# Optimization experiments

Hardware: AMD Instinct MI355X
Metric: run time of the kernel (lower is better)

The kernel has to match this reference:

```python
import jax, jax.numpy as jnp
import numpy as np

B, N, F_ = 4, 2048, 512
H = 8
D = F_ // H


def setup_inputs() -> dict:
    key = jax.random.key(0)
    ks = jax.random.split(key, 9)
    s = 1.0 / np.sqrt(F_)
    return {
        "x": jax.random.normal(ks[0], (B, N, F_), dtype=jnp.float32),
        "Wq": jax.random.normal(ks[1], (F_, F_), dtype=jnp.float32) * s,
        "bq": jax.random.normal(ks[2], (F_,), dtype=jnp.float32) * 0.01,
        "Wk": jax.random.normal(ks[3], (F_, F_), dtype=jnp.float32) * s,
        "bk": jax.random.normal(ks[4], (F_,), dtype=jnp.float32) * 0.01,
        "Wv": jax.random.normal(ks[5], (F_, F_), dtype=jnp.float32) * s,
        "bv": jax.random.normal(ks[6], (F_,), dtype=jnp.float32) * 0.01,
        "Wo": jax.random.normal(ks[7], (F_, F_), dtype=jnp.float32) * s,
        "bo": jax.random.normal(ks[8], (F_,), dtype=jnp.float32) * 0.01,
    }


def reference(x, Wq, bq, Wk, bk, Wv, bv, Wo, bo):
    b, n, f = x.shape
    h, d = H, f // H
    # projections -> [b, h, n, d]
    q = (x @ Wq + bq).reshape(b, n, h, d).transpose(0, 2, 1, 3)
    k = (x @ Wk + bk).reshape(b, n, h, d).transpose(0, 2, 1, 3)
    v = (x @ Wv + bv).reshape(b, n, h, d).transpose(0, 2, 1, 3)
    # NOTE: module scales by sqrt(feats), not sqrt(head_dim)
    sqrt_d = jnp.asarray(f, x.dtype) ** 0.5
    score = jax.nn.softmax(jnp.einsum('bhif,bhjf->bhij', q, k) / sqrt_d, axis=-1)
    attn = jnp.einsum('bhij,bhjf->bihf', score, v).reshape(b, n, f)
    return attn @ Wo + bo
```

## Files before the change

### kernel.cpp

```cpp
#include <hip/hip_runtime.h>


typedef _Float16 f16;
typedef _Float16 f16x2 __attribute__((ext_vector_type(2)));
typedef _Float16 f16x4 __attribute__((ext_vector_type(4)));
typedef _Float16 f16x8 __attribute__((ext_vector_type(8)));
typedef float f32x4 __attribute__((ext_vector_type(4)));

#define MFMA16(a, b, c) __builtin_amdgcn_mfma_f32_16x16x32_f16((a), (b), (c), 0, 0, 0)
#if __has_builtin(__builtin_amdgcn_exp2f)
#define EXP2(x) __builtin_amdgcn_exp2f(x)
#else
#define EXP2(x) exp2f(x)
#endif
#define GLLDS16(gp, lp)                                                    \
  __builtin_amdgcn_global_load_lds(                                        \
      (const __attribute__((address_space(1))) unsigned int*)(gp),         \
      (__attribute__((address_space(3))) unsigned int*)(lp), 16, 0, 0)

#define QSCALE 0.0637587f

__global__ __launch_bounds__(256) void k_cvt_x(const float* __restrict__ x,
                                               f16* __restrict__ xb, int n4) {
  int i = blockIdx.x * 256 + threadIdx.x;
  const int stride = gridDim.x * 256;
  const float4* xp = (const float4*)x;
  f16x4* op = (f16x4*)xb;
  for (; i < n4; i += stride) {
    float4 v = xp[i];
    f16x4 o = {(f16)v.x, (f16)v.y, (f16)v.z, (f16)v.w};
    op[i] = o;
  }
}

__global__ __launch_bounds__(256) void k_cvt_w(const float* __restrict__ Wq,
                                               const float* __restrict__ Wk,
                                               const float* __restrict__ Wv,
                                               const float* __restrict__ Wo,
                                               f16* __restrict__ wt) {
  const int w = blockIdx.y;
  const float* W = (w == 0) ? Wq : (w == 1) ? Wk : (w == 2) ? Wv : Wo;
  const int j0 = (blockIdx.x >> 4) * 32;
  const int k0 = (blockIdx.x & 15) * 32;
  __shared__ float tl[32][33];
  const int tx = threadIdx.x & 31, ty = threadIdx.x >> 5;
#pragma unroll
  for (int i = 0; i < 32; i += 8)
    tl[ty + i][tx] = W[(size_t)(k0 + ty + i) * 512 + j0 + tx];
  __syncthreads();
#pragma unroll
  for (int i = 0; i < 32; i += 8)
    wt[(size_t)w * 262144 + (size_t)(j0 + ty + i) * 512 + (k0 + tx)] =
        (f16)tl[tx][ty + i];
}

__global__ __launch_bounds__(256) void k_gemm(
    const f16* __restrict__ A, const f16* __restrict__ Wb3,
    const float* __restrict__ bias0, const float* __restrict__ bias1,
    const float* __restrict__ bias2, f16* __restrict__ oQ, f16* __restrict__ oK,
    f16* __restrict__ oV, float* __restrict__ oOut, int mode) {
  __shared__ __align__(16) f16 a_lds[128 * 64];
  __shared__ __align__(16) f16 b_lds[128 * 64];
  const int t = threadIdx.x;
  const int lane = t & 63, wid = t >> 6;
  const int l15 = lane & 15, l4 = lane >> 4;
  const int wm = wid >> 1, wn = wid & 1;
  const int m0 = blockIdx.x * 128;
  const int by = blockIdx.y;
  const int wsel = (mode == 0) ? (by >> 2) : 0;
  const int n0l = (mode == 0) ? ((by & 3) * 128) : (by * 128);
  const f16* Wt = Wb3 + (size_t)wsel * 262144;

  const int srow = t >> 3;
  const int sslot = t & 7;
  const int sswz = (sslot ^ (srow & 7)) * 8;

  f32x4 acc[4][4];
  const f32x4 z4 = {0.f, 0.f, 0.f, 0.f};
#pragma unroll
  for (int i = 0; i < 4; i++)
#pragma unroll
    for (int j = 0; j < 4; j++) acc[i][j] = z4;

  for (int k0 = 0; k0 < 512; k0 += 64) {
#pragma unroll
    for (int i = 0; i < 4; i++) {
      const int r = i * 32 + srow;
      *(f16x8*)&a_lds[r * 64 + sslot * 8] =
          *(const f16x8*)&A[(size_t)(m0 + r) * 512 + k0 + sswz];
      *(f16x8*)&b_lds[r * 64 + sslot * 8] =
          *(const f16x8*)&Wt[(size_t)(n0l + r) * 512 + k0 + sswz];
    }
    __syncthreads();
#pragma unroll
    for (int ks = 0; ks < 2; ks++) {
      const int rs = ((ks * 4 + l4) ^ (l15 & 7)) * 8;
      f16x8 af[4], bf[4];
#pragma unroll
      for (int mt = 0; mt < 4; mt++)
        af[mt] = *(const f16x8*)&a_lds[(wm * 64 + mt * 16 + l15) * 64 + rs];
#pragma unroll
      for (int nt = 0; nt < 4; nt++)
        bf[nt] = *(const f16x8*)&b_lds[(wn * 64 + nt * 16 + l15) * 64 + rs];
      __builtin_amdgcn_s_setprio(1);
#pragma unroll
      for (int mt = 0; mt < 4; mt++)
#pragma unroll
        for (int nt = 0; nt < 4; nt++)
          acc[mt][nt] = MFMA16(af[mt], bf[nt], acc[mt][nt]);
      __builtin_amdgcn_s_setprio(0);
    }
    __syncthreads();
  }

  if (mode == 1) {
#pragma unroll
    for (int mt = 0; mt < 4; mt++)
#pragma unroll
      for (int nt = 0; nt < 4; nt++) {
        const int row = m0 + wm * 64 + mt * 16 + l4 * 4;
        const int col = n0l + wn * 64 + nt * 16 + l15;
        const float bv = bias0[col];
#pragma unroll
        for (int r = 0; r < 4; r++)
          oOut[(size_t)(row + r) * 512 + col] = acc[mt][nt][r] + bv;
      }
  } else {
#pragma unroll
    for (int mt = 0; mt < 4; mt++)
#pragma unroll
      for (int nt = 0; nt < 4; nt++) {
        const int colg = by * 128 + wn * 64 + nt * 16 + l15;
        const int w = colg >> 9, jj = colg & 511;
        const int h = jj >> 6, d = jj & 63;
        const float* bp = (w == 0) ? bias0 : (w == 1) ? bias1 : bias2;
        const float bv = bp[jj];
        const float scl = (w == 0) ? QSCALE : 1.0f;
        const int rowg = m0 + wm * 64 + mt * 16 + l4 * 4;
        const int b = rowg >> 11, nn = rowg & 2047;
        if (w == 2) {
          const size_t vb = ((size_t)(b * 8 + h) * 64 + d) * 2048 + nn;
#pragma unroll
          for (int r = 0; r < 4; r++)
            oV[vb + r] = (f16)(acc[mt][nt][r] + bv);
        } else {
          f16* op = (w == 0) ? oQ : oK;
          const size_t base = ((size_t)(b * 8 + h) * 2048 + nn) * 64 + d;
#pragma unroll
          for (int r = 0; r < 4; r++)
            op[base + (size_t)r * 64] = (f16)((acc[mt][nt][r] + bv) * scl);
        }
      }
  }
}

__global__ __launch_bounds__(256, 2) void k_attn(const f16* __restrict__ Q,
                                                 const f16* __restrict__ K,
                                                 const f16* __restrict__ Vt,
                                                 f16* __restrict__ CTX) {
  __shared__ __align__(16) f16 k_lds[2][4096];
  __shared__ __align__(16) f16 v_lds[2][4096];
  const int t = threadIdx.x, wid = t >> 6, lane = t & 63;
  const int l15 = lane & 15, l4 = lane >> 4;
  const int bid = blockIdx.x;
  const int bh = (bid & 7) * 4 + (bid >> 7);
  const int qb = (bid >> 3) & 15;
  const int q0 = qb * 128 + wid * 32;
  const size_t kvb = (size_t)bh * (2048 * 64);

  f16x8 qf[2][2];
#pragma unroll
  for (int g = 0; g < 2; g++)
#pragma unroll
    for (int ks = 0; ks < 2; ks++)
      qf[g][ks] = *(const f16x8*)&Q[kvb + (size_t)(q0 + g * 16 + l15) * 64 +
                                    ks * 32 + l4 * 8];

  f32x4 oa[2][4];
  f32x4 lacc[2];
  const f32x4 z4 = {0.f, 0.f, 0.f, 0.f};
#pragma unroll
  for (int g = 0; g < 2; g++) {
    lacc[g] = z4;
#pragma unroll
    for (int dt = 0; dt < 4; dt++) oa[g][dt] = z4;
  }
  const f16 one = (f16)1.0f;
  const f16x8 ones = {one, one, one, one, one, one, one, one};

  const int krow = wid * 8 + (lane >> 3);
  const int kswz = ((lane & 7) ^ (lane >> 3)) * 8;
  const int kperm = ((krow & 0x0C) << 1) | ((krow & 0x10) >> 2) | (krow & 3);
  const f16* Kg = K + kvb + (size_t)kperm * 64 + kswz;
  const f16* Vg = Vt + kvb + (size_t)krow * 2048 + kswz;

  GLLDS16(Kg, &k_lds[0][wid * 512]);
  GLLDS16(Kg + 2048, &k_lds[0][wid * 512 + 2048]);
  GLLDS16(Vg, &v_lds[0][wid * 512]);
  GLLDS16(Vg + 32 * 2048, &v_lds[0][wid * 512 + 2048]);
  __syncthreads();

  int cur = 0;
  for (int it = 0; it < 32; ++it) {
    if (it < 31) {
      const size_t kb = (size_t)(it + 1) * 4096;
      const size_t vb = (size_t)(it + 1) * 64;
      GLLDS16(Kg + kb, &k_lds[cur ^ 1][wid * 512]);
      GLLDS16(Kg + kb + 2048, &k_lds[cur ^ 1][wid * 512 + 2048]);
      GLLDS16(Vg + vb, &v_lds[cur ^ 1][wid * 512]);
      GLLDS16(Vg + vb + 32 * 2048, &v_lds[cur ^ 1][wid * 512 + 2048]);
    }

    f32x4 st[2][4];
#pragma unroll
    for (int g = 0; g < 2; g++)
#pragma unroll
      for (int w = 0; w < 4; w++) st[g][w] = z4;
    const f16* kl = k_lds[cur];
#pragma unroll
    for (int ks = 0; ks < 2; ks++) {
      const int rs = ((ks * 4 + l4) ^ (l15 & 7)) * 8;
      f16x8 kf[4];
#pragma unroll
      for (int w = 0; w < 4; w++)
        kf[w] = *(const f16x8*)&kl[(w * 16 + l15) * 64 + rs];
      __builtin_amdgcn_s_setprio(1);
#pragma unroll
      for (int w = 0; w < 4; w++) {
        st[0][w] = MFMA16(kf[w], qf[0][ks], st[0][w]);
        st[1][w] = MFMA16(kf[w], qf[1][ks], st[1][w]);
      }
      __builtin_amdgcn_s_setprio(0);
    }

    f16x8 pa[2][2];
#pragma unroll
    for (int g = 0; g < 2; g++)
#pragma unroll
      for (int ks = 0; ks < 2; ks++) {
        f16x2 a0 = __builtin_bit_cast(
            f16x2, __builtin_amdgcn_cvt_pkrtz(EXP2(st[g][2 * ks][0]),
                                              EXP2(st[g][2 * ks][1])));
        f16x2 a1 = __builtin_bit_cast(
            f16x2, __builtin_amdgcn_cvt_pkrtz(EXP2(st[g][2 * ks][2]),
                                              EXP2(st[g][2 * ks][3])));
        f16x2 a2 = __builtin_bit_cast(
            f16x2, __builtin_amdgcn_cvt_pkrtz(EXP2(st[g][2 * ks + 1][0]),
                                              EXP2(st[g][2 * ks + 1][1])));
        f16x2 a3 = __builtin_bit_cast(
            f16x2, __builtin_amdgcn_cvt_pkrtz(EXP2(st[g][2 * ks + 1][2]),
                                              EXP2(st[g][2 * ks + 1][3])));
        f16x8 p;
        p[0] = a0[0]; p[1] = a0[1]; p[2] = a1[0]; p[3] = a1[1];
        p[4] = a2[0]; p[5] = a2[1]; p[6] = a3[0]; p[7] = a3[1];
        pa[g][ks] = p;
      }

    const f16* vl = v_lds[cur];
#pragma unroll
    for (int ks = 0; ks < 2; ks++) {
      __builtin_amdgcn_s_setprio(1);
      lacc[0] = MFMA16(pa[0][ks], ones, lacc[0]);
      lacc[1] = MFMA16(pa[1][ks], ones, lacc[1]);
#pragma unroll
      for (int dt = 0; dt < 4; dt++) {
        const f16x8 vf = *(const f16x8*)&vl[(dt * 16 + l15) * 64 +
                                            ((ks * 4 + l4) ^ (l15 & 7)) * 8];
        oa[0][dt] = MFMA16(pa[0][ks], vf, oa[0][dt]);
        oa[1][dt] = MFMA16(pa[1][ks], vf, oa[1][dt]);
      }
      __builtin_amdgcn_s_setprio(0);
    }
    __syncthreads();
    cur ^= 1;
  }

  const int b = bh >> 3, h = bh & 7;
#pragma unroll
  for (int g = 0; g < 2; g++)
#pragma unroll
    for (int r = 0; r < 4; r++) {
      const float inv = 1.0f / lacc[g][r];
      const int qrow = q0 + g * 16 + l4 * 4 + r;
#pragma unroll
      for (int dt = 0; dt < 4; dt++)
        CTX[(size_t)(b * 2048 + qrow) * 512 + h * 64 + dt * 16 + l15] =
            (f16)(oa[g][dt][r] * inv);
    }
}

extern "C" void kernel_launch(void* const* d_in, const int* in_sizes, int n_in,
                              void* d_out, int out_size, void* d_ws,
                              size_t ws_size, hipStream_t stream) {
  const float* x = (const float*)d_in[0];
  const float* Wq = (const float*)d_in[1];
  const float* bq = (const float*)d_in[2];
  const float* Wk = (const float*)d_in[3];
  const float* bk = (const float*)d_in[4];
  const float* Wv = (const float*)d_in[5];
  const float* bv = (const float*)d_in[6];
  const float* Wo = (const float*)d_in[7];
  const float* bo = (const float*)d_in[8];
  float* out = (float*)d_out;
  char* ws = (char*)d_ws;

  f16* xb = (f16*)(ws);
  f16* wt = (f16*)(ws + (size_t)(8u << 20));
  f16* Qb = (f16*)(ws + (size_t)(10u << 20));
  f16* Kb = (f16*)(ws + (size_t)(18u << 20));
  f16* Vt = (f16*)(ws + (size_t)(26u << 20));
  f16* CX = (f16*)(ws + (size_t)(34u << 20));

  k_cvt_x<<<dim3(2048), dim3(256), 0, stream>>>(x, xb, 1048576);
  k_cvt_w<<<dim3(256, 4), dim3(256), 0, stream>>>(Wq, Wk, Wv, Wo, wt);
  k_gemm<<<dim3(64, 12), dim3(256), 0, stream>>>(xb, wt, bq, bk, bv, Qb, Kb, Vt,
                                                 nullptr, 0);
  k_attn<<<dim3(512), dim3(256), 0, stream>>>(Qb, Kb, Vt, CX);
  k_gemm<<<dim3(64, 4), dim3(256), 0, stream>>>(CX, wt + (size_t)3 * 262144, bo,
                                                nullptr, nullptr, nullptr,
                                                nullptr, nullptr, out, 1);
}
```

Measured before the change: 90.44 us.

## Shrink attention blocks to two waves, async LDS loads in GEMM, narrower output GEMM tiles

```diff
diff --git a/kernel.cpp b/kernel.cpp
--- a/kernel.cpp
+++ b/kernel.cpp
@@ -54,57 +54,59 @@
         (f16)tl[tx][ty + i];
 }
 
+template <int BN, int MODE>
 __global__ __launch_bounds__(256) void k_gemm(
     const f16* __restrict__ A, const f16* __restrict__ Wb3,
     const float* __restrict__ bias0, const float* __restrict__ bias1,
     const float* __restrict__ bias2, f16* __restrict__ oQ, f16* __restrict__ oK,
-    f16* __restrict__ oV, float* __restrict__ oOut, int mode) {
+    f16* __restrict__ oV, float* __restrict__ oOut) {
   __shared__ __align__(16) f16 a_lds[128 * 64];
-  __shared__ __align__(16) f16 b_lds[128 * 64];
+  __shared__ __align__(16) f16 b_lds[BN * 64];
   const int t = threadIdx.x;
   const int lane = t & 63, wid = t >> 6;
   const int l15 = lane & 15, l4 = lane >> 4;
-  const int wm = wid >> 1, wn = wid & 1;
+  constexpr int MT = (BN == 128) ? 4 : 2;
+  const int mbase = (BN == 128) ? (wid >> 1) * 64 : wid * 32;
+  const int nbase = (BN == 128) ? (wid & 1) * 64 : 0;
   const int m0 = blockIdx.x * 128;
   const int by = blockIdx.y;
-  const int wsel = (mode == 0) ? (by >> 2) : 0;
-  const int n0l = (mode == 0) ? ((by & 3) * 128) : (by * 128);
+  const int wsel = (MODE == 0) ? (by >> 2) : 0;
+  const int n0l = (MODE == 0) ? ((by & 3) * 128) : (by * (BN == 64 ? 64 : 128));
   const f16* Wt = Wb3 + (size_t)wsel * 262144;
 
   const int srow = t >> 3;
-  const int sslot = t & 7;
-  const int sswz = (sslot ^ (srow & 7)) * 8;
-
-  f32x4 acc[4][4];
+  const int sswz = ((t & 7) ^ (srow & 7)) * 8;
+  const f16* Ag = A + (size_t)(m0 + srow) * 512 + sswz;
+  const f16* Bg = Wt + (size_t)(n0l + srow) * 512 + sswz;
+
+  f32x4 acc[MT][4];
   const f32x4 z4 = {0.f, 0.f, 0.f, 0.f};
 #pragma unroll
-  for (int i = 0; i < 4; i++)
+  for (int i = 0; i < MT; i++)
 #pragma unroll
     for (int j = 0; j < 4; j++) acc[i][j] = z4;
 
   for (int k0 = 0; k0 < 512; k0 += 64) {
 #pragma unroll
-    for (int i = 0; i < 4; i++) {
-      const int r = i * 32 + srow;
-      *(f16x8*)&a_lds[r * 64 + sslot * 8] =
-          *(const f16x8*)&A[(size_t)(m0 + r) * 512 + k0 + sswz];
-      *(f16x8*)&b_lds[r * 64 + sslot * 8] =
-          *(const f16x8*)&Wt[(size_t)(n0l + r) * 512 + k0 + sswz];
-    }
+    for (int i = 0; i < 4; i++)
+      GLLDS16(Ag + (size_t)i * 16384 + k0, &a_lds[i * 2048 + wid * 512]);
+#pragma unroll
+    for (int i = 0; i < BN / 32; i++)
+      GLLDS16(Bg + (size_t)i * 16384 + k0, &b_lds[i * 2048 + wid * 512]);
     __syncthreads();
 #pragma unroll
     for (int ks = 0; ks < 2; ks++) {
       const int rs = ((ks * 4 + l4) ^ (l15 & 7)) * 8;
-      f16x8 af[4], bf[4];
-#pragma unroll
-      for (int mt = 0; mt < 4; mt++)
-        af[mt] = *(const f16x8*)&a_lds[(wm * 64 + mt * 16 + l15) * 64 + rs];
+      f16x8 af[MT], bf[4];
+#pragma unroll
+      for (int mt = 0; mt < MT; mt++)
+        af[mt] = *(const f16x8*)&a_lds[(mbase + mt * 16 + l15) * 64 + rs];
 #pragma unroll
       for (int nt = 0; nt < 4; nt++)
-        bf[nt] = *(const f16x8*)&b_lds[(wn * 64 + nt * 16 + l15) * 64 + rs];
+        bf[nt] = *(const f16x8*)&b_lds[(nbase + nt * 16 + l15) * 64 + rs];
       __builtin_amdgcn_s_setprio(1);
 #pragma unroll
-      for (int mt = 0; mt < 4; mt++)
+      for (int mt = 0; mt < MT; mt++)
 #pragma unroll
         for (int nt = 0; nt < 4; nt++)
           acc[mt][nt] = MFMA16(af[mt], bf[nt], acc[mt][nt]);
@@ -113,13 +115,13 @@
     __syncthreads();
   }
 
-  if (mode == 1) {
-#pragma unroll
-    for (int mt = 0; mt < 4; mt++)
+  if (MODE == 1) {
+#pragma unroll
+    for (int mt = 0; mt < MT; mt++)
 #pragma unroll
       for (int nt = 0; nt < 4; nt++) {
-        const int row = m0 + wm * 64 + mt * 16 + l4 * 4;
-        const int col = n0l + wn * 64 + nt * 16 + l15;
+        const int row = m0 + mbase + mt * 16 + l4 * 4;
+        const int col = n0l + nbase + nt * 16 + l15;
         const float bv = bias0[col];
 #pragma unroll
         for (int r = 0; r < 4; r++)
@@ -127,16 +129,16 @@
       }
   } else {
 #pragma unroll
-    for (int mt = 0; mt < 4; mt++)
+    for (int mt = 0; mt < MT; mt++)
 #pragma unroll
       for (int nt = 0; nt < 4; nt++) {
-        const int colg = by * 128 + wn * 64 + nt * 16 + l15;
+        const int colg = by * 128 + nbase + nt * 16 + l15;
         const int w = colg >> 9, jj = colg & 511;
         const int h = jj >> 6, d = jj & 63;
         const float* bp = (w == 0) ? bias0 : (w == 1) ? bias1 : bias2;
         const float bv = bp[jj];
         const float scl = (w == 0) ? QSCALE : 1.0f;
-        const int rowg = m0 + wm * 64 + mt * 16 + l4 * 4;
+        const int rowg = m0 + mbase + mt * 16 + l4 * 4;
         const int b = rowg >> 11, nn = rowg & 2047;
         if (w == 2) {
           const size_t vb = ((size_t)(b * 8 + h) * 64 + d) * 2048 + nn;
@@ -154,7 +156,7 @@
   }
 }
 
-__global__ __launch_bounds__(256, 2) void k_attn(const f16* __restrict__ Q,
+__global__ __launch_bounds__(128, 4) void k_attn(const f16* __restrict__ Q,
                                                  const f16* __restrict__ K,
                                                  const f16* __restrict__ Vt,
                                                  f16* __restrict__ CTX) {
@@ -163,9 +165,9 @@
   const int t = threadIdx.x, wid = t >> 6, lane = t & 63;
   const int l15 = lane & 15, l4 = lane >> 4;
   const int bid = blockIdx.x;
-  const int bh = (bid & 7) * 4 + (bid >> 7);
-  const int qb = (bid >> 3) & 15;
-  const int q0 = qb * 128 + wid * 32;
+  const int bh = (bid & 7) * 4 + (bid >> 8);
+  const int qb = (bid >> 3) & 31;
+  const int q0 = qb * 64 + wid * 32;
   const size_t kvb = (size_t)bh * (2048 * 64);
 
   f16x8 qf[2][2];
@@ -188,16 +190,22 @@
   const f16 one = (f16)1.0f;
   const f16x8 ones = {one, one, one, one, one, one, one, one};
 
-  const int krow = wid * 8 + (lane >> 3);
   const int kswz = ((lane & 7) ^ (lane >> 3)) * 8;
-  const int kperm = ((krow & 0x0C) << 1) | ((krow & 0x10) >> 2) | (krow & 3);
-  const f16* Kg = K + kvb + (size_t)kperm * 64 + kswz;
-  const f16* Vg = Vt + kvb + (size_t)krow * 2048 + kswz;
-
-  GLLDS16(Kg, &k_lds[0][wid * 512]);
-  GLLDS16(Kg + 2048, &k_lds[0][wid * 512 + 2048]);
-  GLLDS16(Vg, &v_lds[0][wid * 512]);
-  GLLDS16(Vg + 32 * 2048, &v_lds[0][wid * 512 + 2048]);
+  const f16* Kgp[4];
+  const f16* Vgp[4];
+#pragma unroll
+  for (int i = 0; i < 4; i++) {
+    const int L = i * 16 + wid * 8 + (lane >> 3);
+    const int pr = (L & 0x20) | ((L & 0x0C) << 1) | ((L & 0x10) >> 2) | (L & 3);
+    Kgp[i] = K + kvb + (size_t)pr * 64 + kswz;
+    Vgp[i] = Vt + kvb + (size_t)L * 2048 + kswz;
+  }
+
+#pragma unroll
+  for (int i = 0; i < 4; i++) {
+    GLLDS16(Kgp[i], &k_lds[0][i * 1024 + wid * 512]);
+    GLLDS16(Vgp[i], &v_lds[0][i * 1024 + wid * 512]);
+  }
   __syncthreads();
 
   int cur = 0;
@@ -205,10 +213,11 @@
     if (it < 31) {
       const size_t kb = (size_t)(it + 1) * 4096;
       const size_t vb = (size_t)(it + 1) * 64;
-      GLLDS16(Kg + kb, &k_lds[cur ^ 1][wid * 512]);
-      GLLDS16(Kg + kb + 2048, &k_lds[cur ^ 1][wid * 512 + 2048]);
-      GLLDS16(Vg + vb, &v_lds[cur ^ 1][wid * 512]);
-      GLLDS16(Vg + vb + 32 * 2048, &v_lds[cur ^ 1][wid * 512 + 2048]);
+#pragma unroll
+      for (int i = 0; i < 4; i++) {
+        GLLDS16(Kgp[i] + kb, &k_lds[cur ^ 1][i * 1024 + wid * 512]);
+        GLLDS16(Vgp[i] + vb, &v_lds[cur ^ 1][i * 1024 + wid * 512]);
+      }
     }
 
     f32x4 st[2][4];
@@ -313,10 +322,10 @@
 
   k_cvt_x<<<dim3(2048), dim3(256), 0, stream>>>(x, xb, 1048576);
   k_cvt_w<<<dim3(256, 4), dim3(256), 0, stream>>>(Wq, Wk, Wv, Wo, wt);
-  k_gemm<<<dim3(64, 12), dim3(256), 0, stream>>>(xb, wt, bq, bk, bv, Qb, Kb, Vt,
-                                                 nullptr, 0);
-  k_attn<<<dim3(512), dim3(256), 0, stream>>>(Qb, Kb, Vt, CX);
-  k_gemm<<<dim3(64, 4), dim3(256), 0, stream>>>(CX, wt + (size_t)3 * 262144, bo,
-                                                nullptr, nullptr, nullptr,
-                                                nullptr, nullptr, out, 1);
-}
+  k_gemm<128, 0><<<dim3(64, 12), dim3(256), 0, stream>>>(
+      xb, wt, bq, bk, bv, Qb, Kb, Vt, nullptr);
+  k_attn<<<dim3(1024), dim3(128), 0, stream>>>(Qb, Kb, Vt, CX);
+  k_gemm<64, 1><<<dim3(64, 8), dim3(256), 0, stream>>>(
+      CX, wt + (size_t)3 * 262144, bo, nullptr, nullptr, nullptr, nullptr,
+      nullptr, out);
+}
```

Measured after the change: 96.95 us. 7.2% more time.
